# Kernel tuning notes

Measured on AMD Instinct MI355X. Metric: run time of the kernel, lower is better.

## Reference

```python
import jax, jax.numpy as jnp
import numpy as np

B, S, D, F_INT = 8, 1024, 1024, 4096
N_EDGES = 262144
NUM_REL = 2
LN_EPS = 1e-6


def setup_inputs() -> dict:
    key = jax.random.key(0)
    ks = jax.random.split(key, 10)
    N = B * S
    glorot_w = float(np.sqrt(6.0 / (D + F_INT)))
    glorot_r = float(np.sqrt(6.0 / (D + F_INT)))
    return {
        "hidden_states": jax.random.normal(ks[0], (B, S, D), dtype=jnp.float32),
        "weight": jax.random.uniform(ks[1], (NUM_REL, D, F_INT), jnp.float32, -glorot_w, glorot_w),
        "root": jax.random.uniform(ks[2], (D, F_INT), jnp.float32, -glorot_r, glorot_r),
        "bias": jnp.zeros((F_INT,), jnp.float32),
        "wo": jax.random.normal(ks[3], (F_INT, D), dtype=jnp.float32) * 0.02,
        "ln_gamma": jnp.ones((D,), jnp.float32),
        "ln_beta": jnp.zeros((D,), jnp.float32),
        "edge_index": jax.random.randint(ks[4], (2, N_EDGES), 0, N, dtype=jnp.int32),
        "edge_type": jax.random.randint(ks[5], (N_EDGES,), 0, NUM_REL, dtype=jnp.int32),
    }


def reference(hidden_states, weight, root, bias, wo, ln_gamma, ln_beta, edge_index, edge_type):
    Bz, Sq, Dm = hidden_states.shape
    N = Bz * Sq
    # LayerNorm
    mu = hidden_states.mean(-1, keepdims=True)
    var = jnp.mean((hidden_states - mu) ** 2, axis=-1, keepdims=True)
    norm_x = (hidden_states - mu) * jax.lax.rsqrt(var + LN_EPS) * ln_gamma + ln_beta
    x = norm_x.reshape(N, Dm)  # [N, D] node features

    src, dst = edge_index[0], edge_index[1]
    out = jnp.zeros((N, weight.shape[2]), dtype=x.dtype)
    # RGCNConv: per-relation masked gather -> scatter-mean -> matmul
    for r in range(NUM_REL):
        mask = (edge_type == r)
        msg = jnp.where(mask[:, None], x[src], 0.0)          # [E, D]
        agg = jax.ops.segment_sum(msg, dst, num_segments=N)  # [N, D]
        cnt = jax.ops.segment_sum(mask.astype(x.dtype), dst, num_segments=N)
        h = agg / jnp.maximum(cnt, 1.0)[:, None]             # mean aggr (0 if no edges)
        out = out + h @ weight[r]
    out = out + x @ root + bias
    # relu -> wo -> residual (dropout = identity at eval)
    out = jax.nn.relu(out) @ wo
    return hidden_states + out.reshape(Bz, Sq, Dm)
```

## Files before the change

kernel.cpp:

```cpp
#include <hip/hip_runtime.h>


typedef unsigned short u16;
typedef unsigned int   u32;
typedef __attribute__((ext_vector_type(8))) short bf16x8;
typedef __attribute__((ext_vector_type(4))) float f32x4;
typedef __attribute__((ext_vector_type(2))) float f32x2;

#define E_NUM  262144
#define NNODE  8192
#define NBKT   (2 * NNODE)
#define DDIM   1024
#define FDIM   4096
#define KCAT   3072
#define LN_EPS 1e-6f

struct alignas(8) u16x4 { u16 x, y, z, w; };

__device__ __forceinline__ u16 f2bf(float f) {
  u32 u = __float_as_uint(f);
  u32 r = u + 0x7fffu + ((u >> 16) & 1u);
  return (u16)(r >> 16);
}
__device__ __forceinline__ float bf2f(u16 h) {
  return __uint_as_float(((u32)h) << 16);
}

__device__ __forceinline__ u32 enc_fp8_1(float f) {
  u32 u = __float_as_uint(f);
  u32 s = u >> 31;
  u32 mag = u & 0x7fffffffu;
  mag = mag + 0x7ffffu + ((mag >> 20) & 1u);
  if (mag > 0x43e00000u) mag = 0x43e00000u;
  u32 e = mag >> 23;
  return (e <= 120u) ? 0u
                     : ((s << 7) | ((e - 120u) << 3) | ((mag >> 20) & 7u));
}

__device__ __forceinline__ u32 pack4_fp8(float a, float b, float c, float d) {
#if __has_builtin(__builtin_amdgcn_cvt_pk_fp8_f32)
  int v = 0;
  v = __builtin_amdgcn_cvt_pk_fp8_f32(a, b, v, false);
  v = __builtin_amdgcn_cvt_pk_fp8_f32(c, d, v, true);
  return (u32)v;
#else
  return enc_fp8_1(a) | (enc_fp8_1(b) << 8) | (enc_fp8_1(c) << 16) |
         (enc_fp8_1(d) << 24);
#endif
}

__device__ __forceinline__ float dec_fp8_1(u32 b) {
  u32 e = (b >> 3) & 15u;
  u32 f = ((b & 0x80u) << 24) | ((e + 120u) << 23) | ((b & 7u) << 20);
  return e ? __uint_as_float(f) : 0.0f;
}

__device__ __forceinline__ void acc4_fp8(float* a, u32 q) {
#if __has_builtin(__builtin_amdgcn_cvt_pk_f32_fp8)
  f32x2 p0 = __builtin_amdgcn_cvt_pk_f32_fp8((int)q, false);
  f32x2 p1 = __builtin_amdgcn_cvt_pk_f32_fp8((int)q, true);
  a[0] += p0.x; a[1] += p0.y; a[2] += p1.x; a[3] += p1.y;
#else
  a[0] += dec_fp8_1(q);       a[1] += dec_fp8_1(q >> 8);
  a[2] += dec_fp8_1(q >> 16); a[3] += dec_fp8_1(q >> 24);
#endif
}

__device__ __forceinline__ void acc16_fp8(float* a, uint4 x) {
  acc4_fp8(a + 0,  x.x); acc4_fp8(a + 4,  x.y);
  acc4_fp8(a + 8,  x.z); acc4_fp8(a + 12, x.w);
}

#define GLD16(gp, lp)                                              \
  __builtin_amdgcn_global_load_lds(                                \
      (__attribute__((address_space(1))) u32*)(gp),                \
      (__attribute__((address_space(3))) u32*)(lp), 16, 0, 0)

__global__ void ln_kernel(const float* __restrict__ hs,
                          const float* __restrict__ gamma,
                          const float* __restrict__ beta,
                          u16* __restrict__ hcat,
                          u32* __restrict__ xq,
                          const int* __restrict__ edge_index,
                          const int* __restrict__ edge_type,
                          int* __restrict__ cnt) {
  const int row = blockIdx.x;
  const int tid = threadIdx.x;
  const float4 v = ((const float4*)(hs + (size_t)row * DDIM))[tid];

  if (tid < 32) {
    const int e = (row << 5) + tid;
    const int d = edge_index[E_NUM + e];
    const int r = edge_type[e];
    atomicAdd(&cnt[r * NNODE + d], 1);
  }

  __shared__ float r1[256], r2[256];
  r1[tid] = v.x + v.y + v.z + v.w;
  r2[tid] = v.x * v.x + v.y * v.y + v.z * v.z + v.w * v.w;
  __syncthreads();
  for (int st = 128; st > 0; st >>= 1) {
    if (tid < st) { r1[tid] += r1[tid + st]; r2[tid] += r2[tid + st]; }
    __syncthreads();
  }
  const float mean = r1[0] * (1.0f / DDIM);
  const float var  = r2[0] * (1.0f / DDIM) - mean * mean;
  const float rs   = rsqrtf(var + LN_EPS);

  const int base = tid * 4;
  const float4 g = *(const float4*)(gamma + base);
  const float4 b = *(const float4*)(beta + base);
  const float o0 = (v.x - mean) * rs * g.x + b.x;
  const float o1 = (v.y - mean) * rs * g.y + b.y;
  const float o2 = (v.z - mean) * rs * g.z + b.z;
  const float o3 = (v.w - mean) * rs * g.w + b.w;
  u16x4 o;
  o.x = f2bf(o0); o.y = f2bf(o1); o.z = f2bf(o2); o.w = f2bf(o3);
  *(u16x4*)(hcat + (size_t)row * KCAT + 2048 + base) = o;
  xq[row * 256 + tid] = pack4_fp8(o0, o1, o2, o3);
}

__global__ void cvt_transpose(const float* __restrict__ srcA,
                              const float* __restrict__ srcB,
                              int splitK, int K, int N,
                              u16* __restrict__ dst) {
  __shared__ float tile[32][33];
  const int n0 = blockIdx.x * 32, k0 = blockIdx.y * 32;
  const int tx = threadIdx.x, ty = threadIdx.y;
  for (int i = ty; i < 32; i += 8) {
    const int k = k0 + i;
    const float v = (k < splitK) ? srcA[(size_t)k * N + n0 + tx]
                                 : srcB[(size_t)(k - splitK) * N + n0 + tx];
    tile[i][tx] = v;
  }
  __syncthreads();
  for (int i = ty; i < 32; i += 8) {
    dst[(size_t)(n0 + i) * K + k0 + tx] = f2bf(tile[tx][i]);
  }
}

__global__ __launch_bounds__(1024) void scan_kernel(const int* __restrict__ cnt,
                                                    int* __restrict__ off,
                                                    int* __restrict__ cursor) {
  __shared__ int partial[1024];
  const int tid  = threadIdx.x;
  const int base = tid * 16;
  int local[16];
  int s = 0;
#pragma unroll
  for (int i = 0; i < 16; ++i) { local[i] = s; s += cnt[base + i]; }
  partial[tid] = s;
  __syncthreads();
  for (int st = 1; st < 1024; st <<= 1) {
    const int v = (tid >= st) ? partial[tid - st] : 0;
    __syncthreads();
    partial[tid] += v;
    __syncthreads();
  }
  const int pre = (tid == 0) ? 0 : partial[tid - 1];
#pragma unroll
  for (int i = 0; i < 16; ++i) {
    const int o = pre + local[i];
    off[base + i]    = o;
    cursor[base + i] = o;
  }
}

__global__ void fill_kernel(const int* __restrict__ edge_index,
                            const int* __restrict__ edge_type,
                            int* __restrict__ cursor,
                            int* __restrict__ bucket_src) {
  const int e = blockIdx.x * 256 + threadIdx.x;
  const int s = edge_index[e];
  const int d = edge_index[E_NUM + e];
  const int r = edge_type[e];
  const int pos = atomicAdd(&cursor[r * NNODE + d], 1);
  bucket_src[pos] = s;
}

__global__ __launch_bounds__(256) void aggregate_kernel(
    const int* __restrict__ cnt, const int* __restrict__ off,
    const int* __restrict__ bucket_src, const u32* __restrict__ xq,
    u16* __restrict__ hcat) {
  const int b    = blockIdx.x * 4 + (threadIdx.x >> 6);
  const int lane = threadIdx.x & 63;
  const int r    = b >> 13;
  const int node = b & (NNODE - 1);
  const int n     = cnt[b];
  const int start = off[b];

  float a[16] = {};

  for (int j0 = 0; j0 < n; j0 += 64) {
    const int m = min(n - j0, 64);
    const int myid = (lane < m) ? bucket_src[start + j0 + lane] : 0;
    int j = 0;
    for (; j + 3 < m; j += 4) {
      const int s0 = __shfl(myid, j,     64);
      const int s1 = __shfl(myid, j + 1, 64);
      const int s2 = __shfl(myid, j + 2, 64);
      const int s3 = __shfl(myid, j + 3, 64);
      const uint4 x0 = *(const uint4*)(xq + s0 * 256 + lane * 4);
      const uint4 x1 = *(const uint4*)(xq + s1 * 256 + lane * 4);
      const uint4 x2 = *(const uint4*)(xq + s2 * 256 + lane * 4);
      const uint4 x3 = *(const uint4*)(xq + s3 * 256 + lane * 4);
      acc16_fp8(a, x0); acc16_fp8(a, x1);
      acc16_fp8(a, x2); acc16_fp8(a, x3);
    }
    for (; j < m; ++j) {
      const int s0 = __shfl(myid, j, 64);
      const uint4 x0 = *(const uint4*)(xq + s0 * 256 + lane * 4);
      acc16_fp8(a, x0);
    }
  }

  const float inv = 1.0f / fmaxf((float)n, 1.0f);
  uint4 o0, o1;
  o0.x = (u32)f2bf(a[0] * inv)  | ((u32)f2bf(a[1] * inv)  << 16);
  o0.y = (u32)f2bf(a[2] * inv)  | ((u32)f2bf(a[3] * inv)  << 16);
  o0.z = (u32)f2bf(a[4] * inv)  | ((u32)f2bf(a[5] * inv)  << 16);
  o0.w = (u32)f2bf(a[6] * inv)  | ((u32)f2bf(a[7] * inv)  << 16);
  o1.x = (u32)f2bf(a[8] * inv)  | ((u32)f2bf(a[9] * inv)  << 16);
  o1.y = (u32)f2bf(a[10] * inv) | ((u32)f2bf(a[11] * inv) << 16);
  o1.z = (u32)f2bf(a[12] * inv) | ((u32)f2bf(a[13] * inv) << 16);
  o1.w = (u32)f2bf(a[14] * inv) | ((u32)f2bf(a[15] * inv) << 16);
  u16* dp = hcat + (size_t)node * KCAT + (size_t)r * DDIM + lane * 16;
  *(uint4*)(dp)     = o0;
  *(uint4*)(dp + 8) = o1;
}


#define MF16(a, b, c) __builtin_amdgcn_mfma_f32_16x16x32_bf16(a, b, c, 0, 0, 0)

#define FENCE asm volatile("" ::: "memory")

#define STAGE_A(t, p, b)                                                   \
  { GLD16(gA0 + (size_t)(t) * 64 + (size_t)(p) * KP,                       \
          &sA[b][(p) * 8192 + lofs0]);                                     \
    GLD16(gA1 + (size_t)(t) * 64 + (size_t)(p) * KP,                       \
          &sA[b][(p) * 8192 + lofs1]); }

#define STAGE_B(t, p, b)                                                   \
  { GLD16(gB0 + (size_t)(t) * 64 + (size_t)(p) * KP,                       \
          &sB[b][(p) * 8192 + lofs0]);                                     \
    GLD16(gB1 + (size_t)(t) * 64 + (size_t)(p) * KP,                       \
          &sB[b][(p) * 8192 + lofs1]); }

#define BVLOAD(b)                                                          \
  { const bf16x8* pB_ = (const bf16x8*)sB[b];                              \
    bv[0][0] = pB_[brow80 + sega0]; bv[0][1] = pB_[brow80 + sega1];        \
    bv[1][0] = pB_[brow81 + sega0]; bv[1][1] = pB_[brow81 + sega1];        \
    bv[2][0] = pB_[brow82 + sega0]; bv[2][1] = pB_[brow82 + sega1];        \
    bv[3][0] = pB_[brow83 + sega0]; bv[3][1] = pB_[brow83 + sega1]; }

#define NOWAIT ((void)0)
#define NOSTAGE ((void)0)
#define VM4 asm volatile("s_waitcnt vmcnt(4)" ::: "memory")
#define VM2 asm volatile("s_waitcnt vmcnt(2)" ::: "memory")
#define VM0 asm volatile("s_waitcnt vmcnt(0)" ::: "memory")

#define PHASE(Q, BUFI, STAGE, ENDW)                                        \
  { const bf16x8* pA_ = (const bf16x8*)sA[BUFI];                           \
    bf16x8 a00 = pA_[arow8[2 * (Q)] + sega0];                              \
    bf16x8 a01 = pA_[arow8[2 * (Q)] + sega1];                              \
    bf16x8 a10 = pA_[arow8[2 * (Q) + 1] + sega0];                          \
    bf16x8 a11 = pA_[arow8[2 * (Q) + 1] + sega1];                          \
    STAGE;                                                                 \
    __builtin_amdgcn_s_barrier();                                          \
    FENCE;                                                                 \
    __builtin_amdgcn_s_setprio(1);                                         \
    _Pragma("unroll")                                                      \
    for (int ni = 0; ni < 4; ++ni) {                                       \
      acc[2 * (Q)][ni]     = MF16(a00, bv[ni][0], acc[2 * (Q)][ni]);       \
      acc[2 * (Q)][ni]     = MF16(a01, bv[ni][1], acc[2 * (Q)][ni]);       \
      acc[2 * (Q) + 1][ni] = MF16(a10, bv[ni][0], acc[2 * (Q) + 1][ni]);   \
      acc[2 * (Q) + 1][ni] = MF16(a11, bv[ni][1], acc[2 * (Q) + 1][ni]);   \
    }                                                                      \
    __builtin_amdgcn_s_setprio(0);                                         \
    ENDW;                                                                  \
    __builtin_amdgcn_s_barrier();                                          \
    FENCE; }

__global__ __launch_bounds__(512) void gemm1_kernel(
    const u16* __restrict__ A, const u16* __restrict__ Bt,
    const float* __restrict__ bias, u16* __restrict__ obf) {
  const int K = KCAT, N = FDIM;
  const int NT = K / 64;
  const size_t KP = (size_t)128 * K;
  __shared__ __align__(16) u16 smem[65536];
  u16 (*sA)[16384] = (u16(*)[16384])(smem);
  u16 (*sB)[16384] = (u16(*)[16384])(smem + 32768);

  const int tid  = threadIdx.x;
  const int lane = tid & 63;
  const int wave = tid >> 6;
  const int wr = wave >> 2, wc = wave & 3;
  const int lr = lane & 15, quad = lane >> 4;

  const int bid = blockIdx.x;
  const int swz = (bid & 7) * 64 + (bid >> 3);
  const int bm = (swz >> 4) * 256;
  const int bn = (swz & 15) * 256;

  int lofs0, lofs1;
  const u16 *gA0, *gA1, *gB0, *gB1;
  {
    const int s0 = tid,       r0 = s0 >> 3, g0 = (s0 & 7) ^ (r0 & 7);
    const int s1 = tid + 512, r1 = s1 >> 3, g1 = (s1 & 7) ^ (r1 & 7);
    gA0 = A  + (size_t)(bm + r0) * K + g0 * 8;
    gA1 = A  + (size_t)(bm + r1) * K + g1 * 8;
    gB0 = Bt + (size_t)(bn + r0) * K + g0 * 8;
    gB1 = Bt + (size_t)(bn + r1) * K + g1 * 8;
    lofs0 = s0 * 8; lofs1 = s1 * 8;
  }

  int arow8[8];
#pragma unroll
  for (int mi = 0; mi < 8; ++mi) arow8[mi] = (wr * 128 + mi * 16 + lr) * 8;
  const int brow80 = (wc * 64 +  0 + lr) * 8;
  const int brow81 = (wc * 64 + 16 + lr) * 8;
  const int brow82 = (wc * 64 + 32 + lr) * 8;
  const int brow83 = (wc * 64 + 48 + lr) * 8;
  const int sega0 = quad ^ (lr & 7);
  const int sega1 = (4 + quad) ^ (lr & 7);

  f32x4 acc[8][4] = {};
  bf16x8 bv[4][2];

  STAGE_B(0, 0, 0) STAGE_B(0, 1, 0)
  STAGE_A(0, 0, 0) STAGE_A(0, 1, 0)
  STAGE_B(1, 0, 1) STAGE_B(1, 1, 1)
  asm volatile("s_waitcnt vmcnt(4)" ::: "memory");
  __builtin_amdgcn_s_barrier();
  FENCE;

  for (int tt = 0; tt < NT - 2; tt += 2) {
    PHASE(0, 0, BVLOAD(0); STAGE_A(tt + 1, 0, 1), NOWAIT)
    PHASE(1, 0, STAGE_A(tt + 1, 1, 1), NOWAIT)
    PHASE(2, 0, STAGE_B(tt + 2, 0, 0), NOWAIT)
    PHASE(3, 0, STAGE_B(tt + 2, 1, 0), VM4)
    PHASE(0, 1, BVLOAD(1); STAGE_A(tt + 2, 0, 0), NOWAIT)
    PHASE(1, 1, STAGE_A(tt + 2, 1, 0), NOWAIT)
    PHASE(2, 1, STAGE_B(tt + 3, 0, 1), NOWAIT)
    PHASE(3, 1, STAGE_B(tt + 3, 1, 1), VM4)
  }
  PHASE(0, 0, BVLOAD(0); STAGE_A(NT - 1, 0, 1), NOWAIT)
  PHASE(1, 0, STAGE_A(NT - 1, 1, 1), NOWAIT)
  PHASE(2, 0, NOSTAGE, NOWAIT)
  PHASE(3, 0, NOSTAGE, VM0)
  PHASE(0, 1, BVLOAD(1), NOWAIT)
  PHASE(1, 1, NOSTAGE, NOWAIT)
  PHASE(2, 1, NOSTAGE, NOWAIT)
  PHASE(3, 1, NOSTAGE, NOWAIT)

  const int CPAD = 264;
#pragma unroll
  for (int h = 0; h < 2; ++h) {
    if (wr == h) {
#pragma unroll
      for (int mi = 0; mi < 8; ++mi) {
        const int lrow = mi * 16 + quad * 4;
#pragma unroll
        for (int ni = 0; ni < 4; ++ni) {
          const int col = wc * 64 + ni * 16 + lr;
          const float bb = bias[bn + col];
#pragma unroll
          for (int r = 0; r < 4; ++r) {
            const float v = acc[mi][ni][r] + bb;
            smem[(lrow + r) * CPAD + col] = f2bf(fmaxf(v, 0.0f));
          }
        }
      }
    }
    __syncthreads();
#pragma unroll
    for (int i = 0; i < 8; ++i) {
      const int chunk = tid + 512 * i;
      const int row = chunk >> 5;
      const int seg = chunk & 31;
      const uint4 val = *(const uint4*)(smem + row * CPAD + seg * 8);
      *(uint4*)(obf + (size_t)(bm + h * 128 + row) * N + bn + seg * 8) = val;
    }
    __syncthreads();
  }
}

__global__ __launch_bounds__(512) void gemm2_kernel(
    const u16* __restrict__ A, const u16* __restrict__ Bt,
    const float* __restrict__ resid, float* __restrict__ out) {
  const int K = FDIM, N = DDIM;
  const int NT = K / 64;
  const size_t KP = (size_t)128 * K;
  __shared__ __align__(16) u16 smem[49152];
  u16 (*sA)[16384] = (u16(*)[16384])(smem);
  u16 (*sB)[8192]  = (u16(*)[8192])(smem + 32768);

  const int tid  = threadIdx.x;
  const int lane = tid & 63;
  const int wave = tid >> 6;
  const int wr = wave >> 1, wc = wave & 1;
  const int lr = lane & 15, quad = lane >> 4;

  const int bid = blockIdx.x;
  const int swz = (bid & 7) * 32 + (bid >> 3);
  const int bm = (swz >> 3) * 256;
  const int bn = (swz & 7) * 128;

  int lofs0, lofs1;
  const u16 *gA0, *gA1, *gB0, *gB1;
  {
    const int s0 = tid,       r0 = s0 >> 3, g0 = (s0 & 7) ^ (r0 & 7);
    const int s1 = tid + 512, r1 = s1 >> 3, g1 = (s1 & 7) ^ (r1 & 7);
    gA0 = A  + (size_t)(bm + r0) * K + g0 * 8;
    gA1 = A  + (size_t)(bm + r1) * K + g1 * 8;
    gB0 = Bt + (size_t)(bn + r0) * K + g0 * 8;
    gB1 = Bt + (size_t)(bn + r1) * K + g1 * 8;
    lofs0 = s0 * 8; lofs1 = s1 * 8;
  }

  int arow8[4];
#pragma unroll
  for (int mi = 0; mi < 4; ++mi) arow8[mi] = (wr * 64 + mi * 16 + lr) * 8;
  const int brow80 = (wc * 64 +  0 + lr) * 8;
  const int brow81 = (wc * 64 + 16 + lr) * 8;
  const int brow82 = (wc * 64 + 32 + lr) * 8;
  const int brow83 = (wc * 64 + 48 + lr) * 8;
  const int sega0 = quad ^ (lr & 7);
  const int sega1 = (4 + quad) ^ (lr & 7);

  f32x4 acc[4][4] = {};
  bf16x8 bv[4][2];

  STAGE_B(0, 0, 0)
  STAGE_A(0, 0, 0) STAGE_A(0, 1, 0)
  STAGE_B(1, 0, 1)
  asm volatile("s_waitcnt vmcnt(2)" ::: "memory");
  __builtin_amdgcn_s_barrier();
  FENCE;

  for (int tt = 0; tt < NT - 2; tt += 2) {
    PHASE(0, 0, BVLOAD(0); STAGE_A(tt + 1, 0, 1), NOWAIT)
    PHASE(1, 0, STAGE_A(tt + 1, 1, 1); STAGE_B(tt + 2, 0, 0), VM2)
    PHASE(0, 1, BVLOAD(1); STAGE_A(tt + 2, 0, 0), NOWAIT)
    PHASE(1, 1, STAGE_A(tt + 2, 1, 0); STAGE_B(tt + 3, 0, 1), VM2)
  }
  PHASE(0, 0, BVLOAD(0); STAGE_A(NT - 1, 0, 1), NOWAIT)
  PHASE(1, 0, STAGE_A(NT - 1, 1, 1), VM0)
  PHASE(0, 1, BVLOAD(1), NOWAIT)
  PHASE(1, 1, NOSTAGE, NOWAIT)

  float* smemf = (float*)smem;
  const int FPAD = 132;
#pragma unroll
  for (int h = 0; h < 2; ++h) {
    __syncthreads();
    if ((wr >> 1) == h) {
#pragma unroll
      for (int mi = 0; mi < 4; ++mi) {
        const int srow0 = (wr & 1) * 64 + mi * 16 + quad * 4;
#pragma unroll
        for (int ni = 0; ni < 4; ++ni) {
          const int scol = wc * 64 + ni * 16 + lr;
#pragma unroll
          for (int r = 0; r < 4; ++r)
            smemf[(srow0 + r) * FPAD + scol] = acc[mi][ni][r];
        }
      }
    }
    __syncthreads();
#pragma unroll
    for (int i = 0; i < 8; ++i) {
      const int chunk = tid + 512 * i;
      const int row = chunk >> 5;
      const int seg = chunk & 31;
      const float4 lv = *(const float4*)(smemf + row * FPAD + seg * 4);
      const size_t gofs = (size_t)(bm + h * 128 + row) * N + bn + seg * 4;
      const float4 rv = *(const float4*)(resid + gofs);
      float4 ov;
      ov.x = rv.x + lv.x; ov.y = rv.y + lv.y;
      ov.z = rv.z + lv.z; ov.w = rv.w + lv.w;
      *(float4*)(out + gofs) = ov;
    }
  }
}

extern "C" void kernel_launch(void* const* d_in, const int* in_sizes, int n_in,
                              void* d_out, int out_size, void* d_ws, size_t ws_size,
                              hipStream_t stream) {
  const float* hs     = (const float*)d_in[0];
  const float* weight = (const float*)d_in[1];
  const float* root   = (const float*)d_in[2];
  const float* bias   = (const float*)d_in[3];
  const float* wo     = (const float*)d_in[4];
  const float* gamma  = (const float*)d_in[5];
  const float* beta   = (const float*)d_in[6];
  const int* edge_index = (const int*)d_in[7];
  const int* edge_type  = (const int*)d_in[8];
  float* out = (float*)d_out;

  char* ws = (char*)d_ws;
  u16*   hcat       = (u16*)(ws + 0);
  u16*   WcatT      = (u16*)(ws + 50331648);
  u16*   woT        = (u16*)(ws + 75497472);
  u16*   out1       = (u16*)(ws + 83886080);
  int*   bucket_src = (int*)(ws + 83886080);
  int*   cnt        = (int*)(ws + 84934656);
  int*   off        = (int*)(ws + 85000192);
  int*   cursor     = (int*)(ws + 85065728);
  u32*   xq         = (u32*)(ws + 85131264);

  (void)hipMemsetAsync(cnt, 0, 65536, stream);

  ln_kernel<<<NNODE, 256, 0, stream>>>(hs, gamma, beta, hcat, xq,
                                       edge_index, edge_type, cnt);

  scan_kernel<<<1, 1024, 0, stream>>>(cnt, off, cursor);
  fill_kernel<<<E_NUM / 256, 256, 0, stream>>>(edge_index, edge_type, cursor, bucket_src);
  aggregate_kernel<<<NBKT / 4, 256, 0, stream>>>(cnt, off, bucket_src, xq, hcat);

  cvt_transpose<<<dim3(FDIM / 32, KCAT / 32), dim3(32, 8), 0, stream>>>(
      weight, root, 2048, KCAT, FDIM, WcatT);
  cvt_transpose<<<dim3(DDIM / 32, FDIM / 32), dim3(32, 8), 0, stream>>>(
      wo, wo, FDIM, FDIM, DDIM, woT);

  gemm1_kernel<<<512, 512, 0, stream>>>(hcat, WcatT, bias, out1);

  gemm2_kernel<<<256, 512, 0, stream>>>(out1, woT, hs, out);
}
```

Before: 459.2 us.

## Fuse aggregation with weight convert-transpose kernels and software-pipeline gather loads

Merges the fp8 neighbor aggregation and both weight fp32-to-bf16 transpose kernels into one launch, with block index ranges selecting the role, so the small latency-bound gather can overlap with the bandwidth-bound weight conversion and two launches go away. The gather loop now uses readlane instead of shuffles for the source index, double-buffers four rows of loads ahead of accumulation, and accumulates in packed float2 to allow packed adds. The trade-offs are higher register pressure and shared LDS allocated even by aggregation blocks, which could lower occupancy.

```diff
diff --git a/kernel.cpp b/kernel.cpp
--- a/kernel.cpp
+++ b/kernel.cpp
@@ -14,6 +14,10 @@
 #define FDIM   4096
 #define KCAT   3072
 #define LN_EPS 1e-6f
+
+#define AGG_BLOCKS  (NBKT / 4)
+#define CVT1_BLOCKS ((FDIM / 32) * (KCAT / 32))
+#define CVT2_BLOCKS ((DDIM / 32) * (FDIM / 32))
 
 struct alignas(8) u16x4 { u16 x, y, z, w; };
 
@@ -55,20 +59,24 @@
   return e ? __uint_as_float(f) : 0.0f;
 }
 
-__device__ __forceinline__ void acc4_fp8(float* a, u32 q) {
+template <bool HI>
+__device__ __forceinline__ f32x2 cvt2_fp8(u32 q) {
 #if __has_builtin(__builtin_amdgcn_cvt_pk_f32_fp8)
-  f32x2 p0 = __builtin_amdgcn_cvt_pk_f32_fp8((int)q, false);
-  f32x2 p1 = __builtin_amdgcn_cvt_pk_f32_fp8((int)q, true);
-  a[0] += p0.x; a[1] += p0.y; a[2] += p1.x; a[3] += p1.y;
+  return __builtin_amdgcn_cvt_pk_f32_fp8((int)q, HI);
 #else
-  a[0] += dec_fp8_1(q);       a[1] += dec_fp8_1(q >> 8);
-  a[2] += dec_fp8_1(q >> 16); a[3] += dec_fp8_1(q >> 24);
+  f32x2 r;
+  const u32 sh = HI ? 16u : 0u;
+  r.x = dec_fp8_1((q >> sh) & 0xffu);
+  r.y = dec_fp8_1((q >> (sh + 8)) & 0xffu);
+  return r;
 #endif
 }
 
-__device__ __forceinline__ void acc16_fp8(float* a, uint4 x) {
-  acc4_fp8(a + 0,  x.x); acc4_fp8(a + 4,  x.y);
-  acc4_fp8(a + 8,  x.z); acc4_fp8(a + 12, x.w);
+__device__ __forceinline__ void acc16q(f32x2* ac, uint4 q) {
+  ac[0] += cvt2_fp8<false>(q.x); ac[1] += cvt2_fp8<true>(q.x);
+  ac[2] += cvt2_fp8<false>(q.y); ac[3] += cvt2_fp8<true>(q.y);
+  ac[4] += cvt2_fp8<false>(q.z); ac[5] += cvt2_fp8<true>(q.z);
+  ac[6] += cvt2_fp8<false>(q.w); ac[7] += cvt2_fp8<true>(q.w);
 }
 
 #define GLD16(gp, lp)                                              \
@@ -120,25 +128,6 @@
   xq[row * 256 + tid] = pack4_fp8(o0, o1, o2, o3);
 }
 
-__global__ void cvt_transpose(const float* __restrict__ srcA,
-                              const float* __restrict__ srcB,
-                              int splitK, int K, int N,
-                              u16* __restrict__ dst) {
-  __shared__ float tile[32][33];
-  const int n0 = blockIdx.x * 32, k0 = blockIdx.y * 32;
-  const int tx = threadIdx.x, ty = threadIdx.y;
-  for (int i = ty; i < 32; i += 8) {
-    const int k = k0 + i;
-    const float v = (k < splitK) ? srcA[(size_t)k * N + n0 + tx]
-                                 : srcB[(size_t)(k - splitK) * N + n0 + tx];
-    tile[i][tx] = v;
-  }
-  __syncthreads();
-  for (int i = ty; i < 32; i += 8) {
-    dst[(size_t)(n0 + i) * K + k0 + tx] = f2bf(tile[tx][i]);
-  }
-}
-
 __global__ __launch_bounds__(1024) void scan_kernel(const int* __restrict__ cnt,
                                                     int* __restrict__ off,
                                                     int* __restrict__ cursor) {
@@ -178,52 +167,92 @@
   bucket_src[pos] = s;
 }
 
-__global__ __launch_bounds__(256) void aggregate_kernel(
+__device__ __forceinline__ void cvt_body(const float* __restrict__ srcA,
+                                         const float* __restrict__ srcB,
+                                         int splitK, int K, int N,
+                                         u16* __restrict__ dst,
+                                         int n0, int k0, int tx, int ty,
+                                         float (*tile)[33]) {
+  for (int i = ty; i < 32; i += 8) {
+    const int k = k0 + i;
+    const float v = (k < splitK) ? srcA[(size_t)k * N + n0 + tx]
+                                 : srcB[(size_t)(k - splitK) * N + n0 + tx];
+    tile[i][tx] = v;
+  }
+  __syncthreads();
+  for (int i = ty; i < 32; i += 8) {
+    dst[(size_t)(n0 + i) * K + k0 + tx] = f2bf(tile[tx][i]);
+  }
+}
+
+__global__ __launch_bounds__(256) void agg_cvt_kernel(
     const int* __restrict__ cnt, const int* __restrict__ off,
     const int* __restrict__ bucket_src, const u32* __restrict__ xq,
-    u16* __restrict__ hcat) {
-  const int b    = blockIdx.x * 4 + (threadIdx.x >> 6);
-  const int lane = threadIdx.x & 63;
+    u16* __restrict__ hcat,
+    const float* __restrict__ weight, const float* __restrict__ root,
+    u16* __restrict__ WcatT,
+    const float* __restrict__ wo, u16* __restrict__ woT) {
+  __shared__ float tile[32][33];
+  const int bx  = blockIdx.x;
+  const int tid = threadIdx.x;
+
+  if (bx >= AGG_BLOCKS) {
+    const int tx = tid & 31, ty = tid >> 5;
+    if (bx < AGG_BLOCKS + CVT1_BLOCKS) {
+      const int idx = bx - AGG_BLOCKS;
+      cvt_body(weight, root, 2048, KCAT, FDIM, WcatT,
+               (idx & 127) * 32, (idx >> 7) * 32, tx, ty, tile);
+    } else {
+      const int idx = bx - AGG_BLOCKS - CVT1_BLOCKS;
+      cvt_body(wo, wo, FDIM, FDIM, DDIM, woT,
+               (idx & 31) * 32, (idx >> 5) * 32, tx, ty, tile);
+    }
+    return;
+  }
+
+  const int b    = bx * 4 + (tid >> 6);
+  const int lane = tid & 63;
   const int r    = b >> 13;
   const int node = b & (NNODE - 1);
   const int n     = cnt[b];
   const int start = off[b];
 
-  float a[16] = {};
+  f32x2 ac[8] = {};
+
+#define LDROW(j) (*(const uint4*)(xq +                                     \
+    (size_t)__builtin_amdgcn_readlane(myid, (j)) * 256 + lane * 4))
 
   for (int j0 = 0; j0 < n; j0 += 64) {
     const int m = min(n - j0, 64);
     const int myid = (lane < m) ? bucket_src[start + j0 + lane] : 0;
-    int j = 0;
-    for (; j + 3 < m; j += 4) {
-      const int s0 = __shfl(myid, j,     64);
-      const int s1 = __shfl(myid, j + 1, 64);
-      const int s2 = __shfl(myid, j + 2, 64);
-      const int s3 = __shfl(myid, j + 3, 64);
-      const uint4 x0 = *(const uint4*)(xq + s0 * 256 + lane * 4);
-      const uint4 x1 = *(const uint4*)(xq + s1 * 256 + lane * 4);
-      const uint4 x2 = *(const uint4*)(xq + s2 * 256 + lane * 4);
-      const uint4 x3 = *(const uint4*)(xq + s3 * 256 + lane * 4);
-      acc16_fp8(a, x0); acc16_fp8(a, x1);
-      acc16_fp8(a, x2); acc16_fp8(a, x3);
-    }
-    for (; j < m; ++j) {
-      const int s0 = __shfl(myid, j, 64);
-      const uint4 x0 = *(const uint4*)(xq + s0 * 256 + lane * 4);
-      acc16_fp8(a, x0);
-    }
-  }
+    const int nb = m & ~3;
+    if (nb) {
+      uint4 c0 = LDROW(0), c1 = LDROW(1), c2 = LDROW(2), c3 = LDROW(3);
+      for (int j = 4; j < nb; j += 4) {
+        const uint4 t0 = LDROW(j),     t1 = LDROW(j + 1);
+        const uint4 t2 = LDROW(j + 2), t3 = LDROW(j + 3);
+        acc16q(ac, c0); acc16q(ac, c1); acc16q(ac, c2); acc16q(ac, c3);
+        c0 = t0; c1 = t1; c2 = t2; c3 = t3;
+      }
+      acc16q(ac, c0); acc16q(ac, c1); acc16q(ac, c2); acc16q(ac, c3);
+    }
+    for (int j = nb; j < m; ++j) {
+      const uint4 x0 = LDROW(j);
+      acc16q(ac, x0);
+    }
+  }
+#undef LDROW
 
   const float inv = 1.0f / fmaxf((float)n, 1.0f);
   uint4 o0, o1;
-  o0.x = (u32)f2bf(a[0] * inv)  | ((u32)f2bf(a[1] * inv)  << 16);
-  o0.y = (u32)f2bf(a[2] * inv)  | ((u32)f2bf(a[3] * inv)  << 16);
-  o0.z = (u32)f2bf(a[4] * inv)  | ((u32)f2bf(a[5] * inv)  << 16);
-  o0.w = (u32)f2bf(a[6] * inv)  | ((u32)f2bf(a[7] * inv)  << 16);
-  o1.x = (u32)f2bf(a[8] * inv)  | ((u32)f2bf(a[9] * inv)  << 16);
-  o1.y = (u32)f2bf(a[10] * inv) | ((u32)f2bf(a[11] * inv) << 16);
-  o1.z = (u32)f2bf(a[12] * inv) | ((u32)f2bf(a[13] * inv) << 16);
-  o1.w = (u32)f2bf(a[14] * inv) | ((u32)f2bf(a[15] * inv) << 16);
+  o0.x = (u32)f2bf(ac[0].x * inv) | ((u32)f2bf(ac[0].y * inv) << 16);
+  o0.y = (u32)f2bf(ac[1].x * inv) | ((u32)f2bf(ac[1].y * inv) << 16);
+  o0.z = (u32)f2bf(ac[2].x * inv) | ((u32)f2bf(ac[2].y * inv) << 16);
+  o0.w = (u32)f2bf(ac[3].x * inv) | ((u32)f2bf(ac[3].y * inv) << 16);
+  o1.x = (u32)f2bf(ac[4].x * inv) | ((u32)f2bf(ac[4].y * inv) << 16);
+  o1.y = (u32)f2bf(ac[5].x * inv) | ((u32)f2bf(ac[5].y * inv) << 16);
+  o1.z = (u32)f2bf(ac[6].x * inv) | ((u32)f2bf(ac[6].y * inv) << 16);
+  o1.w = (u32)f2bf(ac[7].x * inv) | ((u32)f2bf(ac[7].y * inv) << 16);
   u16* dp = hcat + (size_t)node * KCAT + (size_t)r * DDIM + lane * 16;
   *(uint4*)(dp)     = o0;
   *(uint4*)(dp + 8) = o1;
@@ -516,12 +545,9 @@
 
   scan_kernel<<<1, 1024, 0, stream>>>(cnt, off, cursor);
   fill_kernel<<<E_NUM / 256, 256, 0, stream>>>(edge_index, edge_type, cursor, bucket_src);
-  aggregate_kernel<<<NBKT / 4, 256, 0, stream>>>(cnt, off, bucket_src, xq, hcat);
-
-  cvt_transpose<<<dim3(FDIM / 32, KCAT / 32), dim3(32, 8), 0, stream>>>(
-      weight, root, 2048, KCAT, FDIM, WcatT);
-  cvt_transpose<<<dim3(DDIM / 32, FDIM / 32), dim3(32, 8), 0, stream>>>(
-      wo, wo, FDIM, FDIM, DDIM, woT);
+
+  agg_cvt_kernel<<<AGG_BLOCKS + CVT1_BLOCKS + CVT2_BLOCKS, 256, 0, stream>>>(
+      cnt, off, bucket_src, xq, hcat, weight, root, WcatT, wo, woT);
 
   gemm1_kernel<<<512, 512, 0, stream>>>(hcat, WcatT, bias, out1);
 
```

Result: no change. 452.8 us (-1.4%).
